# Optimization experiments

Measured on AMD Instinct MI355X. Metric: run time of the kernel, lower is better.

The kernel has to match this reference:

```python
import jax, jax.numpy as jnp
import numpy as np

H = 16      # num_attention_heads
D = 64      # attention_head_size
HID = H * D # hidden_size = 1024
N = 1024    # seq_len == max_len
K = 1024    # position_buckets == att_span (K >= N so un-clamped indices stay in range)
EPS = 1e-7  # layer_norm_eps


def setup_inputs() -> dict:
    key = jax.random.key(0)
    ks = jax.random.split(key, 12)

    def w(k, shape):
        return jax.random.normal(k, shape, dtype=jnp.float32) * 0.02

    return {
        "hidden_states": jax.random.normal(ks[0], (1, N, HID), dtype=jnp.float32),
        "rel_embeddings": jax.random.normal(ks[1], (2 * K, HID), dtype=jnp.float32),
        "Wq": w(ks[2], (HID, HID)), "bq": jnp.zeros((HID,), jnp.float32),
        "Wk": w(ks[3], (HID, HID)), "bk": jnp.zeros((HID,), jnp.float32),
        "Wv": w(ks[4], (HID, HID)), "bv": jnp.zeros((HID,), jnp.float32),
        "Wpk": w(ks[5], (HID, HID)), "bpk": jnp.zeros((HID,), jnp.float32),
        "Wpq": w(ks[6], (HID, HID)), "bpq": jnp.zeros((HID,), jnp.float32),
        "Wo": w(ks[7], (HID, HID)), "bo": jnp.zeros((HID,), jnp.float32),
        "ln_g": jnp.ones((HID,), jnp.float32),
        "ln_b": jnp.zeros((HID,), jnp.float32),
    }


def _heads(x):
    # (L, HID) -> (H, L, D)   (batch size is 1, matching the baked-in id offsets)
    L = x.shape[0]
    return x.reshape(L, H, D).transpose(1, 0, 2)


def reference(hidden_states, rel_embeddings, Wq, bq, Wk, bk, Wv, bv,
              Wpk, bpk, Wpq, bpq, Wo, bo, ln_g, ln_b):
    hs = hidden_states[0]                       # (N, HID)
    q = _heads(hs @ Wq.T + bq)                  # (H, N, D)
    k = _heads(hs @ Wk.T + bk)                  # (H, N, D)
    v = _heads(hs @ Wv.T + bv)                  # (H, N, D)

    scale = jnp.sqrt(jnp.asarray(D * 3, jnp.float32))  # scale_factor = 1 + c2p + p2c = 3
    scores = jnp.einsum('hid,hjd->hij', q, k) / scale  # (H, N, N)

    pos_k = _heads(rel_embeddings @ Wpk.T + bpk)       # (H, 2K, D)
    pos_q = _heads(rel_embeddings @ Wpq.T + bpq)       # (H, 2K, D)

    rows = jnp.arange(N)[:, None]                      # (N, 1)
    # ids[i, j] = (i - j) + K  (no clamp in the original; valid since K >= N)
    idx = K + jnp.arange(N)[:, None] - jnp.arange(N)[None, :]  # (N, N)

    # c2p: gather c2p_att[h, i, K + i - j]
    c2p_att = jnp.einsum('hid,hkd->hik', q, pos_k)     # (H, N, 2K)
    c2p = c2p_att[:, rows, idx]                        # (H, N, N)

    # p2c: gather p2c_att[h, i, K + j - i], then transpose last two dims
    p2c_att = jnp.einsum('hid,hkd->hik', k, pos_q)     # (H, N, 2K)
    p2c = jnp.swapaxes(p2c_att[:, rows, idx.T], -1, -2)  # (H, N, N)

    scores = scores + (c2p + p2c) / scale
    attn = jax.nn.softmax(scores, axis=-1)             # (H, N, N)

    ctx = jnp.einsum('hij,hjd->hid', attn, v)          # (H, N, D)
    ctx = ctx.transpose(1, 0, 2).reshape(1, N, HID)    # (1, N, HID)

    # DebertaV2SelfOutput: dense + residual LayerNorm
    out = ctx @ Wo.T + bo
    x = out + hidden_states
    mu = jnp.mean(x, axis=-1, keepdims=True)
    var = jnp.mean(jnp.square(x - mu), axis=-1, keepdims=True)
    return ((x - mu) / jnp.sqrt(var + EPS)) * ln_g + ln_b
```

## Files before the change

### kernel.cpp

```cpp
#include <hip/hip_runtime.h>
#include <stdint.h>

#define HID 1024
#define NSEQ 1024
#define KREL 1024
#define NHEAD 16
#define DHEAD 64

typedef __attribute__((ext_vector_type(8))) short bhalf8;
typedef __attribute__((ext_vector_type(4))) float floatx4;

__device__ inline uint16_t f2bf(float f) {
  union { float f; uint32_t u; } c; c.f = f;
  uint32_t u = c.u;
  return (uint16_t)((u + 0x7fffu + ((u >> 16) & 1u)) >> 16);
}
__device__ inline uint32_t pkbf(float a, float b) {
  union { float f; uint32_t u; } x, y; x.f = a; y.f = b;
#if __has_builtin(__builtin_amdgcn_perm)
  return __builtin_amdgcn_perm(x.u + 0x8000u, y.u + 0x8000u, 0x03020706u);
#else
  return ((x.u + 0x8000u) >> 16) | ((y.u + 0x8000u) & 0xffff0000u);
#endif
}

struct ProjArgs {
  const float* A[5];
  const float* W[5];
  const float* bias[5];
  uint16_t* C[5];
  int trans[5];
};
__global__ __launch_bounds__(256) void proj_gemm(ProjArgs pa) {
  __shared__ uint16_t a_s[2][128 * 40];
  __shared__ uint16_t b_s[2][64 * 40];
  int bidx = blockIdx.x;
  int xcd = bidx & 7, idx = bidx >> 3;
  int gl = idx >> 4, nt = idx & 15;
  int g = xcd * 7 + gl;
  int z, mt;
  if (g < 24) { z = g >> 3; mt = g & 7; }
  else { int g2 = g - 24; z = 3 + (g2 >> 4); mt = g2 & 15; }
  const float* A = pa.A[z];
  const float* W = pa.W[z];
  int i0 = mt * 128, n0 = nt * 64;

  int t = threadIdx.x;
  int lane = t & 63, w = t >> 6;
  int fm = lane & 15, kq = lane >> 4;
  int wrow = w * 32;

  int ra = t >> 1, ca = (t & 1) * 16;
  int rb = t >> 2, cbc = (t & 3) * 8;
  const float* Ap = A + (size_t)(i0 + ra) * HID + ca;
  const float* Wp = W + (size_t)(n0 + rb) * HID + cbc;

  floatx4 acc[2][4] = {};

  float4 fa0 = *(const float4*)(Ap);
  float4 fa1 = *(const float4*)(Ap + 4);
  float4 fa2 = *(const float4*)(Ap + 8);
  float4 fa3 = *(const float4*)(Ap + 12);
  float4 fb0 = *(const float4*)(Wp);
  float4 fb1 = *(const float4*)(Wp + 4);
  {
    uint4 u0 = { pkbf(fa0.x,fa0.y), pkbf(fa0.z,fa0.w), pkbf(fa1.x,fa1.y), pkbf(fa1.z,fa1.w) };
    uint4 u1 = { pkbf(fa2.x,fa2.y), pkbf(fa2.z,fa2.w), pkbf(fa3.x,fa3.y), pkbf(fa3.z,fa3.w) };
    *(uint4*)(&a_s[0][ra * 40 + ca]) = u0;
    *(uint4*)(&a_s[0][ra * 40 + ca + 8]) = u1;
    uint4 ub = { pkbf(fb0.x,fb0.y), pkbf(fb0.z,fb0.w), pkbf(fb1.x,fb1.y), pkbf(fb1.z,fb1.w) };
    *(uint4*)(&b_s[0][rb * 40 + cbc]) = ub;
  }

  for (int kt = 0; kt < 32; ++kt) {
    __syncthreads();
    int cur = kt & 1;
    if (kt < 31) {
      int ko = (kt + 1) * 32;
      fa0 = *(const float4*)(Ap + ko);
      fa1 = *(const float4*)(Ap + ko + 4);
      fa2 = *(const float4*)(Ap + ko + 8);
      fa3 = *(const float4*)(Ap + ko + 12);
      fb0 = *(const float4*)(Wp + ko);
      fb1 = *(const float4*)(Wp + ko + 4);
    }
    const uint16_t* as = &a_s[cur][0];
    const uint16_t* bs = &b_s[cur][0];
    bhalf8 af[2], bfr[4];
#pragma unroll
    for (int m2 = 0; m2 < 2; ++m2)
      af[m2] = *(bhalf8*)(as + (wrow + m2 * 16 + fm) * 40 + kq * 8);
#pragma unroll
    for (int n2 = 0; n2 < 4; ++n2)
      bfr[n2] = *(bhalf8*)(bs + (n2 * 16 + fm) * 40 + kq * 8);
#pragma unroll
    for (int m2 = 0; m2 < 2; ++m2)
#pragma unroll
      for (int n2 = 0; n2 < 4; ++n2)
        acc[m2][n2] = __builtin_amdgcn_mfma_f32_16x16x32_bf16(af[m2], bfr[n2], acc[m2][n2], 0, 0, 0);
    if (kt < 31) {
      int nxt = cur ^ 1;
      uint4 u0 = { pkbf(fa0.x,fa0.y), pkbf(fa0.z,fa0.w), pkbf(fa1.x,fa1.y), pkbf(fa1.z,fa1.w) };
      uint4 u1 = { pkbf(fa2.x,fa2.y), pkbf(fa2.z,fa2.w), pkbf(fa3.x,fa3.y), pkbf(fa3.z,fa3.w) };
      *(uint4*)(&a_s[nxt][ra * 40 + ca]) = u0;
      *(uint4*)(&a_s[nxt][ra * 40 + ca + 8]) = u1;
      uint4 ub = { pkbf(fb0.x,fb0.y), pkbf(fb0.z,fb0.w), pkbf(fb1.x,fb1.y), pkbf(fb1.z,fb1.w) };
      *(uint4*)(&b_s[nxt][rb * 40 + cbc]) = ub;
    }
  }

  const float* bias = pa.bias[z];
  uint16_t* C = pa.C[z];
  int tr = pa.trans[z];
#pragma unroll
  for (int m2 = 0; m2 < 2; ++m2) {
    int rowb = i0 + wrow + m2 * 16 + kq * 4;
#pragma unroll
    for (int n2 = 0; n2 < 4; ++n2) {
      int col = n0 + n2 * 16 + fm;
      float bv = bias[col];
      floatx4 v = acc[m2][n2];
      if (tr) {
        uint2 p = { pkbf(v[0] + bv, v[1] + bv), pkbf(v[2] + bv, v[3] + bv) };
        *(uint2*)(C + (size_t)col * NSEQ + rowb) = p;
      } else {
#pragma unroll
        for (int r = 0; r < 4; ++r)
          C[(size_t)(rowb + r) * HID + col] = f2bf(v[r] + bv);
      }
    }
  }
}

__global__ __launch_bounds__(256) void out_gemm(const uint16_t* __restrict__ Abf,
                                                const float* __restrict__ W,
                                                const float* __restrict__ bias,
                                                float* __restrict__ C) {
  __shared__ uint16_t a_s[2][128 * 40];
  __shared__ uint16_t b_s[2][64 * 40];
  int bidx = blockIdx.x;
  int mt = bidx >> 4, nt = bidx & 15;
  int i0 = mt * 128, n0 = nt * 64;
  int t = threadIdx.x;
  int lane = t & 63, w = t >> 6;
  int fm = lane & 15, kq = lane >> 4;
  int wrow = w * 32;
  int ra = t >> 1, ca = (t & 1) * 16;
  int rb = t >> 2, cbc = (t & 3) * 8;
  const uint16_t* Ap = Abf + (size_t)(i0 + ra) * HID + ca;
  const float* Wp = W + (size_t)(n0 + rb) * HID + cbc;
  floatx4 acc[2][4] = {};
  uint4 va0 = *(const uint4*)(Ap);
  uint4 va1 = *(const uint4*)(Ap + 8);
  float4 fb0 = *(const float4*)(Wp);
  float4 fb1 = *(const float4*)(Wp + 4);
  *(uint4*)(&a_s[0][ra * 40 + ca]) = va0;
  *(uint4*)(&a_s[0][ra * 40 + ca + 8]) = va1;
  {
    uint4 ub = { pkbf(fb0.x,fb0.y), pkbf(fb0.z,fb0.w), pkbf(fb1.x,fb1.y), pkbf(fb1.z,fb1.w) };
    *(uint4*)(&b_s[0][rb * 40 + cbc]) = ub;
  }
  for (int kt = 0; kt < 32; ++kt) {
    __syncthreads();
    int cur = kt & 1;
    if (kt < 31) {
      int ko = (kt + 1) * 32;
      va0 = *(const uint4*)(Ap + ko);
      va1 = *(const uint4*)(Ap + ko + 8);
      fb0 = *(const float4*)(Wp + ko);
      fb1 = *(const float4*)(Wp + ko + 4);
    }
    const uint16_t* as = &a_s[cur][0];
    const uint16_t* bs = &b_s[cur][0];
    bhalf8 af[2], bfr[4];
#pragma unroll
    for (int m2 = 0; m2 < 2; ++m2)
      af[m2] = *(bhalf8*)(as + (wrow + m2 * 16 + fm) * 40 + kq * 8);
#pragma unroll
    for (int n2 = 0; n2 < 4; ++n2)
      bfr[n2] = *(bhalf8*)(bs + (n2 * 16 + fm) * 40 + kq * 8);
#pragma unroll
    for (int m2 = 0; m2 < 2; ++m2)
#pragma unroll
      for (int n2 = 0; n2 < 4; ++n2)
        acc[m2][n2] = __builtin_amdgcn_mfma_f32_16x16x32_bf16(af[m2], bfr[n2], acc[m2][n2], 0, 0, 0);
    if (kt < 31) {
      int nxt = cur ^ 1;
      *(uint4*)(&a_s[nxt][ra * 40 + ca]) = va0;
      *(uint4*)(&a_s[nxt][ra * 40 + ca + 8]) = va1;
      uint4 ub = { pkbf(fb0.x,fb0.y), pkbf(fb0.z,fb0.w), pkbf(fb1.x,fb1.y), pkbf(fb1.z,fb1.w) };
      *(uint4*)(&b_s[nxt][rb * 40 + cbc]) = ub;
    }
  }
#pragma unroll
  for (int m2 = 0; m2 < 2; ++m2) {
    int rowb = i0 + wrow + m2 * 16 + kq * 4;
#pragma unroll
    for (int n2 = 0; n2 < 4; ++n2) {
      int col = n0 + n2 * 16 + fm;
      float bv = bias[col];
#pragma unroll
      for (int r = 0; r < 4; ++r)
        C[(size_t)(rowb + r) * HID + col] = acc[m2][n2][r] + bv;
    }
  }
}

__global__ __launch_bounds__(256) void attn_kernel(const uint16_t* __restrict__ qg,
                                                   const uint16_t* __restrict__ kg,
                                                   const uint16_t* __restrict__ vtg,
                                                   const uint16_t* __restrict__ pkg,
                                                   const uint16_t* __restrict__ pqg,
                                                   uint16_t* __restrict__ ctx) {
  const float RSCALE = 0.07216878364870323f;
  __shared__ uint16_t Qs[32][72];
  __shared__ uint16_t Ks[32][72];
  __shared__ uint16_t Vt[64][40];
  __shared__ uint16_t PKw[64][72];
  __shared__ uint16_t PQw[64][72];
  __shared__ float C2P[32][68];
  __shared__ float P2C[32][68];
  __shared__ float Sqk[32][36];
  __shared__ uint16_t Pbf[32][40];
  __shared__ float m_sm[32], l_sm[32], al_sm[32];

  int t = threadIdx.x;
  int lane = t & 63, w = t >> 6;
  int fm = lane & 15;
  int kq = lane >> 4;

  int b = blockIdx.x;
  int xcd = b & 7, slot = b >> 3;
  int h = xcd * 2 + (slot & 1);
  int i0 = (slot >> 1) * 32;
  int cb = h * DHEAD;

  {
    int r = t >> 3, chq = (t & 7) * 8;
    *(uint4*)(&Qs[r][chq]) = *(const uint4*)(qg + (size_t)(i0 + r) * HID + cb + chq);
  }
  if (t < 32) { m_sm[t] = -1e30f; l_sm[t] = 0.f; }

  floatx4 opv0 = {0,0,0,0}, opv1 = {0,0,0,0};
  int wn = w * 16;
  int smt = w >> 1, snt = w & 1;
  int i2 = t >> 3, jj = t & 7;

  int pr = t >> 3, pch = (t & 7) * 8;
  int rV = t >> 2, cV = (t & 3) * 8;
  const uint16_t* kb = kg + cb + pch;
  const uint16_t* vb = vtg + (size_t)(cb + rV) * HID + cV;
  const uint16_t* pkb = pkg + cb + pch;
  const uint16_t* pqb = pqg + cb + pch;

  uint4 rk, rv, rpk0, rpk1, rpq0, rpq1;
  {
    int j0 = 0;
    int rbase = KREL + i0 - j0 - 31;
    rk = *(const uint4*)(kb + (size_t)(j0 + pr) * HID);
    rv = *(const uint4*)(vb + j0);
    int rg0 = rbase + pr;
    int rg1 = rbase + pr + 32; if (rg1 > 2047) rg1 = 2047;
    rpk0 = *(const uint4*)(pkb + (size_t)rg0 * HID);
    rpk1 = *(const uint4*)(pkb + (size_t)rg1 * HID);
    rpq0 = *(const uint4*)(pqb + (size_t)rg0 * HID);
    rpq1 = *(const uint4*)(pqb + (size_t)rg1 * HID);
  }

  for (int jt = 0; jt < NSEQ / 32; ++jt) {
    __syncthreads();
    *(uint4*)(&Ks[pr][pch]) = rk;
    *(uint4*)(&Vt[rV][cV]) = rv;
    *(uint4*)(&PKw[pr][pch]) = rpk0;
    *(uint4*)(&PKw[pr + 32][pch]) = rpk1;
    *(uint4*)(&PQw[pr][pch]) = rpq0;
    *(uint4*)(&PQw[pr + 32][pch]) = rpq1;
    __syncthreads();

    if (jt + 1 < NSEQ / 32) {
      int j0 = (jt + 1) * 32;
      int rbase = KREL + i0 - j0 - 31;
      rk = *(const uint4*)(kb + (size_t)(j0 + pr) * HID);
      rv = *(const uint4*)(vb + j0);
      int rg0 = rbase + pr; if (rg0 < 0) rg0 = 0;
      int rg1 = rbase + pr + 32; if (rg1 > 2047) rg1 = 2047;
      rpk0 = *(const uint4*)(pkb + (size_t)rg0 * HID);
      rpk1 = *(const uint4*)(pkb + (size_t)rg1 * HID);
      rpq0 = *(const uint4*)(pqb + (size_t)rg0 * HID);
      rpq1 = *(const uint4*)(pqb + (size_t)rg1 * HID);
    }

    {
      const uint16_t* Asrc = (w < 2) ? &Qs[0][0] : &Ks[0][0];
      const uint16_t* Bsrc = (w < 2) ? &PKw[0][0] : &PQw[0][0];
      float* Cdst = (w < 2) ? &C2P[0][0] : &P2C[0][0];
      int ntb = (w & 1) * 2;
#pragma unroll
      for (int mt = 0; mt < 2; ++mt) {
        bhalf8 a0 = *(bhalf8*)(Asrc + (mt * 16 + fm) * 72 + kq * 8);
        bhalf8 a1 = *(bhalf8*)(Asrc + (mt * 16 + fm) * 72 + kq * 8 + 32);
#pragma unroll
        for (int nt = ntb; nt < ntb + 2; ++nt) {
          bhalf8 b0 = *(bhalf8*)(Bsrc + (nt * 16 + fm) * 72 + kq * 8);
          bhalf8 b1 = *(bhalf8*)(Bsrc + (nt * 16 + fm) * 72 + kq * 8 + 32);
          floatx4 acc = {0,0,0,0};
          acc = __builtin_amdgcn_mfma_f32_16x16x32_bf16(a0, b0, acc, 0, 0, 0);
          acc = __builtin_amdgcn_mfma_f32_16x16x32_bf16(a1, b1, acc, 0, 0, 0);
#pragma unroll
          for (int r = 0; r < 4; ++r)
            Cdst[(mt * 16 + kq * 4 + r) * 68 + nt * 16 + fm] = acc[r];
        }
      }
      bhalf8 qa0 = *(bhalf8*)(&Qs[smt * 16 + fm][kq * 8]);
      bhalf8 qa1 = *(bhalf8*)(&Qs[smt * 16 + fm][kq * 8 + 32]);
      bhalf8 kb0 = *(bhalf8*)(&Ks[snt * 16 + fm][kq * 8]);
      bhalf8 kb1 = *(bhalf8*)(&Ks[snt * 16 + fm][kq * 8 + 32]);
      floatx4 sacc = {0,0,0,0};
      sacc = __builtin_amdgcn_mfma_f32_16x16x32_bf16(qa0, kb0, sacc, 0, 0, 0);
      sacc = __builtin_amdgcn_mfma_f32_16x16x32_bf16(qa1, kb1, sacc, 0, 0, 0);
#pragma unroll
      for (int r = 0; r < 4; ++r)
        Sqk[smt * 16 + kq * 4 + r][snt * 16 + fm] = sacc[r];
    }
    __syncthreads();

    {
      float sv[4];
#pragma unroll
      for (int q = 0; q < 4; ++q) {
        int j = jj + 8 * q;
        int rr = i2 - j + 31;
        sv[q] = (Sqk[i2][j] + C2P[i2][rr] + P2C[j][rr]) * RSCALE;
      }
      float mx = fmaxf(fmaxf(sv[0], sv[1]), fmaxf(sv[2], sv[3]));
      mx = fmaxf(mx, __shfl_xor(mx, 1));
      mx = fmaxf(mx, __shfl_xor(mx, 2));
      mx = fmaxf(mx, __shfl_xor(mx, 4));
      float m_old = m_sm[i2];
      float m_new = fmaxf(m_old, mx);
      float al = __expf(m_old - m_new);
      float ts = 0.f;
#pragma unroll
      for (int q = 0; q < 4; ++q) {
        float e = __expf(sv[q] - m_new);
        Pbf[i2][jj + 8 * q] = f2bf(e);
        ts += e;
      }
      ts += __shfl_xor(ts, 1);
      ts += __shfl_xor(ts, 2);
      ts += __shfl_xor(ts, 4);
      if (jj == 0) { m_sm[i2] = m_new; l_sm[i2] = l_sm[i2] * al + ts; al_sm[i2] = al; }
    }
    __syncthreads();

    {
#pragma unroll
      for (int r = 0; r < 4; ++r) {
        opv0[r] *= al_sm[kq * 4 + r];
        opv1[r] *= al_sm[16 + kq * 4 + r];
      }
      bhalf8 vbf = *(bhalf8*)(&Vt[wn + fm][kq * 8]);
      bhalf8 pa0 = *(bhalf8*)(&Pbf[fm][kq * 8]);
      bhalf8 pa1 = *(bhalf8*)(&Pbf[16 + fm][kq * 8]);
      opv0 = __builtin_amdgcn_mfma_f32_16x16x32_bf16(pa0, vbf, opv0, 0, 0, 0);
      opv1 = __builtin_amdgcn_mfma_f32_16x16x32_bf16(pa1, vbf, opv1, 0, 0, 0);
    }
  }

#pragma unroll
  for (int r = 0; r < 4; ++r) {
    int ia = kq * 4 + r, ib = 16 + kq * 4 + r;
    float la = 1.0f / l_sm[ia], lb = 1.0f / l_sm[ib];
    ctx[(size_t)(i0 + ia) * HID + cb + wn + fm] = f2bf(opv0[r] * la);
    ctx[(size_t)(i0 + ib) * HID + cb + wn + fm] = f2bf(opv1[r] * lb);
  }
}

__global__ __launch_bounds__(256) void ln_kernel(const float* __restrict__ xin,
                                                 const float* __restrict__ hs,
                                                 const float* __restrict__ g,
                                                 const float* __restrict__ b,
                                                 float* __restrict__ y) {
  int row = blockIdx.x, t = threadIdx.x;
  int c = t * 4;
  float4 a = *(const float4*)(xin + (size_t)row * HID + c);
  float4 hv = *(const float4*)(hs + (size_t)row * HID + c);
  float x0 = a.x + hv.x, x1 = a.y + hv.y, x2 = a.z + hv.z, x3 = a.w + hv.w;
  float s = x0 + x1 + x2 + x3;
  float sq = x0 * x0 + x1 * x1 + x2 * x2 + x3 * x3;
  for (int off = 32; off; off >>= 1) {
    s += __shfl_xor(s, off);
    sq += __shfl_xor(sq, off);
  }
  __shared__ float rs[4], rq[4];
  int w = t >> 6, lane = t & 63;
  if (lane == 0) { rs[w] = s; rq[w] = sq; }
  __syncthreads();
  s = rs[0] + rs[1] + rs[2] + rs[3];
  sq = rq[0] + rq[1] + rq[2] + rq[3];
  float mu = s * (1.0f / HID);
  float var = sq * (1.0f / HID) - mu * mu;
  float rstd = rsqrtf(var + 1e-7f);
  float4 gg = *(const float4*)(g + c);
  float4 bb = *(const float4*)(b + c);
  float4 out;
  out.x = (x0 - mu) * rstd * gg.x + bb.x;
  out.y = (x1 - mu) * rstd * gg.y + bb.y;
  out.z = (x2 - mu) * rstd * gg.z + bb.z;
  out.w = (x3 - mu) * rstd * gg.w + bb.w;
  *(float4*)(y + (size_t)row * HID + c) = out;
}

extern "C" void kernel_launch(void* const* d_in, const int* in_sizes, int n_in,
                              void* d_out, int out_size, void* d_ws, size_t ws_size,
                              hipStream_t stream) {
  const float* hs  = (const float*)d_in[0];
  const float* rel = (const float*)d_in[1];
  const float* Wq  = (const float*)d_in[2];  const float* bq  = (const float*)d_in[3];
  const float* Wk  = (const float*)d_in[4];  const float* bk  = (const float*)d_in[5];
  const float* Wv  = (const float*)d_in[6];  const float* bv  = (const float*)d_in[7];
  const float* Wpk = (const float*)d_in[8];  const float* bpk = (const float*)d_in[9];
  const float* Wpq = (const float*)d_in[10]; const float* bpq = (const float*)d_in[11];
  const float* Wo  = (const float*)d_in[12]; const float* bo  = (const float*)d_in[13];
  const float* lng = (const float*)d_in[14]; const float* lnb = (const float*)d_in[15];

  char* ws = (char*)d_ws;
  const size_t MB = 1024 * 1024;
  uint16_t* q_bf   = (uint16_t*)(ws + 0 * MB);
  uint16_t* k_bf   = (uint16_t*)(ws + 2 * MB);
  uint16_t* vt_bf  = (uint16_t*)(ws + 4 * MB);
  uint16_t* pk_bf  = (uint16_t*)(ws + 6 * MB);
  uint16_t* pq_bf  = (uint16_t*)(ws + 10 * MB);
  uint16_t* ctx_bf = (uint16_t*)(ws + 14 * MB);
  float*    out_f  = (float*)   (ws + 16 * MB);

  dim3 blk(256);

  ProjArgs pa;
  pa.A[0] = hs;  pa.A[1] = hs;  pa.A[2] = hs;  pa.A[3] = rel; pa.A[4] = rel;
  pa.W[0] = Wq;  pa.W[1] = Wk;  pa.W[2] = Wv;  pa.W[3] = Wpk; pa.W[4] = Wpq;
  pa.bias[0] = bq;  pa.bias[1] = bk;  pa.bias[2] = bv;  pa.bias[3] = bpk; pa.bias[4] = bpq;
  pa.C[0] = q_bf; pa.C[1] = k_bf; pa.C[2] = vt_bf; pa.C[3] = pk_bf; pa.C[4] = pq_bf;
  pa.trans[0] = 0; pa.trans[1] = 0; pa.trans[2] = 1; pa.trans[3] = 0; pa.trans[4] = 0;
  proj_gemm<<<dim3(896), blk, 0, stream>>>(pa);

  attn_kernel<<<dim3(512), blk, 0, stream>>>(q_bf, k_bf, vt_bf, pk_bf, pq_bf, ctx_bf);

  out_gemm<<<dim3(128), blk, 0, stream>>>(ctx_bf, Wo, bo, out_f);

  ln_kernel<<<dim3(1024), blk, 0, stream>>>(out_f, hs, lng, lnb, (float*)d_out);
}
```

Baseline: 235.7 us.

## Pre-cast inputs and weights to bf16, retile out_gemm, store rel-pos scores in bf16

Adds one cast kernel that converts hidden states, rel embeddings and all six weight matrices to bf16 in workspace, so the projection and output GEMMs load bf16 directly instead of converting fp32 in their inner loops. The output GEMM is retiled to 64x64 blocks with a 2x2 warp layout, doubling its grid from 128 to 256 blocks. The attention kernel keeps C2P/P2C tiles in bf16 shared memory, halving that LDS footprint. The extra cast pass adds a launch and about 40MB of memory traffic every call, and the bf16 position scores lose precision.

```diff
diff --git a/kernel.cpp b/kernel.cpp
--- a/kernel.cpp
+++ b/kernel.cpp
@@ -10,6 +10,9 @@
 typedef __attribute__((ext_vector_type(8))) short bhalf8;
 typedef __attribute__((ext_vector_type(4))) float floatx4;
 
+__device__ inline float bf2f(uint16_t h) {
+  union { uint32_t u; float f; } c; c.u = ((uint32_t)h) << 16; return c.f;
+}
 __device__ inline uint16_t f2bf(float f) {
   union { float f; uint32_t u; } c; c.f = f;
   uint32_t u = c.u;
@@ -24,9 +27,27 @@
 #endif
 }
 
+struct Cast8 {
+  const float* src[8];
+  uint16_t* dst[8];
+  int n[8];
+};
+__global__ __launch_bounds__(256) void cast8_kernel(Cast8 c) {
+  int seg = blockIdx.y;
+  int n = c.n[seg];
+  const float* s = c.src[seg];
+  uint16_t* d = c.dst[seg];
+  for (int idx = (blockIdx.x * 256 + threadIdx.x) * 4; idx < n; idx += 1024 * 256 * 4) {
+    float4 v = *(const float4*)(s + idx);
+    ushort4 o;
+    o.x = f2bf(v.x); o.y = f2bf(v.y); o.z = f2bf(v.z); o.w = f2bf(v.w);
+    *(ushort4*)(d + idx) = o;
+  }
+}
+
 struct ProjArgs {
-  const float* A[5];
-  const float* W[5];
+  const uint16_t* A[5];
+  const uint16_t* W[5];
   const float* bias[5];
   uint16_t* C[5];
   int trans[5];
@@ -41,8 +62,8 @@
   int z, mt;
   if (g < 24) { z = g >> 3; mt = g & 7; }
   else { int g2 = g - 24; z = 3 + (g2 >> 4); mt = g2 & 15; }
-  const float* A = pa.A[z];
-  const float* W = pa.W[z];
+  const uint16_t* A = pa.A[z];
+  const uint16_t* W = pa.W[z];
   int i0 = mt * 128, n0 = nt * 64;
 
   int t = threadIdx.x;
@@ -52,37 +73,26 @@
 
   int ra = t >> 1, ca = (t & 1) * 16;
   int rb = t >> 2, cbc = (t & 3) * 8;
-  const float* Ap = A + (size_t)(i0 + ra) * HID + ca;
-  const float* Wp = W + (size_t)(n0 + rb) * HID + cbc;
+  const uint16_t* Ap = A + (size_t)(i0 + ra) * HID + ca;
+  const uint16_t* Wp = W + (size_t)(n0 + rb) * HID + cbc;
 
   floatx4 acc[2][4] = {};
 
-  float4 fa0 = *(const float4*)(Ap);
-  float4 fa1 = *(const float4*)(Ap + 4);
-  float4 fa2 = *(const float4*)(Ap + 8);
-  float4 fa3 = *(const float4*)(Ap + 12);
-  float4 fb0 = *(const float4*)(Wp);
-  float4 fb1 = *(const float4*)(Wp + 4);
-  {
-    uint4 u0 = { pkbf(fa0.x,fa0.y), pkbf(fa0.z,fa0.w), pkbf(fa1.x,fa1.y), pkbf(fa1.z,fa1.w) };
-    uint4 u1 = { pkbf(fa2.x,fa2.y), pkbf(fa2.z,fa2.w), pkbf(fa3.x,fa3.y), pkbf(fa3.z,fa3.w) };
-    *(uint4*)(&a_s[0][ra * 40 + ca]) = u0;
-    *(uint4*)(&a_s[0][ra * 40 + ca + 8]) = u1;
-    uint4 ub = { pkbf(fb0.x,fb0.y), pkbf(fb0.z,fb0.w), pkbf(fb1.x,fb1.y), pkbf(fb1.z,fb1.w) };
-    *(uint4*)(&b_s[0][rb * 40 + cbc]) = ub;
-  }
+  uint4 ua0 = *(const uint4*)(Ap);
+  uint4 ua1 = *(const uint4*)(Ap + 8);
+  uint4 ub = *(const uint4*)(Wp);
+  *(uint4*)(&a_s[0][ra * 40 + ca]) = ua0;
+  *(uint4*)(&a_s[0][ra * 40 + ca + 8]) = ua1;
+  *(uint4*)(&b_s[0][rb * 40 + cbc]) = ub;
 
   for (int kt = 0; kt < 32; ++kt) {
     __syncthreads();
     int cur = kt & 1;
     if (kt < 31) {
       int ko = (kt + 1) * 32;
-      fa0 = *(const float4*)(Ap + ko);
-      fa1 = *(const float4*)(Ap + ko + 4);
-      fa2 = *(const float4*)(Ap + ko + 8);
-      fa3 = *(const float4*)(Ap + ko + 12);
-      fb0 = *(const float4*)(Wp + ko);
-      fb1 = *(const float4*)(Wp + ko + 4);
+      ua0 = *(const uint4*)(Ap + ko);
+      ua1 = *(const uint4*)(Ap + ko + 8);
+      ub = *(const uint4*)(Wp + ko);
     }
     const uint16_t* as = &a_s[cur][0];
     const uint16_t* bs = &b_s[cur][0];
@@ -100,11 +110,8 @@
         acc[m2][n2] = __builtin_amdgcn_mfma_f32_16x16x32_bf16(af[m2], bfr[n2], acc[m2][n2], 0, 0, 0);
     if (kt < 31) {
       int nxt = cur ^ 1;
-      uint4 u0 = { pkbf(fa0.x,fa0.y), pkbf(fa0.z,fa0.w), pkbf(fa1.x,fa1.y), pkbf(fa1.z,fa1.w) };
-      uint4 u1 = { pkbf(fa2.x,fa2.y), pkbf(fa2.z,fa2.w), pkbf(fa3.x,fa3.y), pkbf(fa3.z,fa3.w) };
-      *(uint4*)(&a_s[nxt][ra * 40 + ca]) = u0;
-      *(uint4*)(&a_s[nxt][ra * 40 + ca + 8]) = u1;
-      uint4 ub = { pkbf(fb0.x,fb0.y), pkbf(fb0.z,fb0.w), pkbf(fb1.x,fb1.y), pkbf(fb1.z,fb1.w) };
+      *(uint4*)(&a_s[nxt][ra * 40 + ca]) = ua0;
+      *(uint4*)(&a_s[nxt][ra * 40 + ca + 8]) = ua1;
       *(uint4*)(&b_s[nxt][rb * 40 + cbc]) = ub;
     }
   }
@@ -133,77 +140,61 @@
 }
 
 __global__ __launch_bounds__(256) void out_gemm(const uint16_t* __restrict__ Abf,
-                                                const float* __restrict__ W,
+                                                const uint16_t* __restrict__ W,
                                                 const float* __restrict__ bias,
                                                 float* __restrict__ C) {
-  __shared__ uint16_t a_s[2][128 * 40];
+  __shared__ uint16_t a_s[2][64 * 40];
   __shared__ uint16_t b_s[2][64 * 40];
   int bidx = blockIdx.x;
-  int mt = bidx >> 4, nt = bidx & 15;
-  int i0 = mt * 128, n0 = nt * 64;
+  int i0 = (bidx >> 4) * 64, n0 = (bidx & 15) * 64;
   int t = threadIdx.x;
   int lane = t & 63, w = t >> 6;
   int fm = lane & 15, kq = lane >> 4;
-  int wrow = w * 32;
-  int ra = t >> 1, ca = (t & 1) * 16;
-  int rb = t >> 2, cbc = (t & 3) * 8;
+  int wm = (w >> 1) * 32, wn = (w & 1) * 32;
+  int ra = t >> 2, ca = (t & 3) * 8;
   const uint16_t* Ap = Abf + (size_t)(i0 + ra) * HID + ca;
-  const float* Wp = W + (size_t)(n0 + rb) * HID + cbc;
-  floatx4 acc[2][4] = {};
-  uint4 va0 = *(const uint4*)(Ap);
-  uint4 va1 = *(const uint4*)(Ap + 8);
-  float4 fb0 = *(const float4*)(Wp);
-  float4 fb1 = *(const float4*)(Wp + 4);
-  *(uint4*)(&a_s[0][ra * 40 + ca]) = va0;
-  *(uint4*)(&a_s[0][ra * 40 + ca + 8]) = va1;
-  {
-    uint4 ub = { pkbf(fb0.x,fb0.y), pkbf(fb0.z,fb0.w), pkbf(fb1.x,fb1.y), pkbf(fb1.z,fb1.w) };
-    *(uint4*)(&b_s[0][rb * 40 + cbc]) = ub;
-  }
+  const uint16_t* Wp = W + (size_t)(n0 + ra) * HID + ca;
+  floatx4 acc00 = {0,0,0,0}, acc01 = {0,0,0,0}, acc10 = {0,0,0,0}, acc11 = {0,0,0,0};
+  uint4 ua = *(const uint4*)(Ap);
+  uint4 ub = *(const uint4*)(Wp);
+  *(uint4*)(&a_s[0][ra * 40 + ca]) = ua;
+  *(uint4*)(&b_s[0][ra * 40 + ca]) = ub;
   for (int kt = 0; kt < 32; ++kt) {
     __syncthreads();
     int cur = kt & 1;
     if (kt < 31) {
       int ko = (kt + 1) * 32;
-      va0 = *(const uint4*)(Ap + ko);
-      va1 = *(const uint4*)(Ap + ko + 8);
-      fb0 = *(const float4*)(Wp + ko);
-      fb1 = *(const float4*)(Wp + ko + 4);
+      ua = *(const uint4*)(Ap + ko);
+      ub = *(const uint4*)(Wp + ko);
     }
     const uint16_t* as = &a_s[cur][0];
     const uint16_t* bs = &b_s[cur][0];
-    bhalf8 af[2], bfr[4];
-#pragma unroll
-    for (int m2 = 0; m2 < 2; ++m2)
-      af[m2] = *(bhalf8*)(as + (wrow + m2 * 16 + fm) * 40 + kq * 8);
-#pragma unroll
-    for (int n2 = 0; n2 < 4; ++n2)
-      bfr[n2] = *(bhalf8*)(bs + (n2 * 16 + fm) * 40 + kq * 8);
-#pragma unroll
-    for (int m2 = 0; m2 < 2; ++m2)
-#pragma unroll
-      for (int n2 = 0; n2 < 4; ++n2)
-        acc[m2][n2] = __builtin_amdgcn_mfma_f32_16x16x32_bf16(af[m2], bfr[n2], acc[m2][n2], 0, 0, 0);
+    bhalf8 a0 = *(bhalf8*)(as + (wm + fm) * 40 + kq * 8);
+    bhalf8 a1 = *(bhalf8*)(as + (wm + 16 + fm) * 40 + kq * 8);
+    bhalf8 b0 = *(bhalf8*)(bs + (wn + fm) * 40 + kq * 8);
+    bhalf8 b1 = *(bhalf8*)(bs + (wn + 16 + fm) * 40 + kq * 8);
+    acc00 = __builtin_amdgcn_mfma_f32_16x16x32_bf16(a0, b0, acc00, 0, 0, 0);
+    acc01 = __builtin_amdgcn_mfma_f32_16x16x32_bf16(a0, b1, acc01, 0, 0, 0);
+    acc10 = __builtin_amdgcn_mfma_f32_16x16x32_bf16(a1, b0, acc10, 0, 0, 0);
+    acc11 = __builtin_amdgcn_mfma_f32_16x16x32_bf16(a1, b1, acc11, 0, 0, 0);
     if (kt < 31) {
       int nxt = cur ^ 1;
-      *(uint4*)(&a_s[nxt][ra * 40 + ca]) = va0;
-      *(uint4*)(&a_s[nxt][ra * 40 + ca + 8]) = va1;
-      uint4 ub = { pkbf(fb0.x,fb0.y), pkbf(fb0.z,fb0.w), pkbf(fb1.x,fb1.y), pkbf(fb1.z,fb1.w) };
-      *(uint4*)(&b_s[nxt][rb * 40 + cbc]) = ub;
-    }
-  }
-#pragma unroll
-  for (int m2 = 0; m2 < 2; ++m2) {
-    int rowb = i0 + wrow + m2 * 16 + kq * 4;
-#pragma unroll
-    for (int n2 = 0; n2 < 4; ++n2) {
-      int col = n0 + n2 * 16 + fm;
-      float bv = bias[col];
-#pragma unroll
-      for (int r = 0; r < 4; ++r)
-        C[(size_t)(rowb + r) * HID + col] = acc[m2][n2][r] + bv;
-    }
-  }
+      *(uint4*)(&a_s[nxt][ra * 40 + ca]) = ua;
+      *(uint4*)(&b_s[nxt][ra * 40 + ca]) = ub;
+    }
+  }
+  int rb0 = kq * 4;
+#define EPO(ACC, SM, SN)                                                   \
+  {                                                                        \
+    int rowb = i0 + wm + (SM)*16 + rb0;                                    \
+    int col = n0 + wn + (SN)*16 + fm;                                      \
+    float bv_ = bias[col];                                                 \
+    _Pragma("unroll")                                                      \
+    for (int rr = 0; rr < 4; ++rr)                                         \
+      C[(size_t)(rowb + rr) * HID + col] = ACC[rr] + bv_;                  \
+  }
+  EPO(acc00, 0, 0) EPO(acc01, 0, 1) EPO(acc10, 1, 0) EPO(acc11, 1, 1)
+#undef EPO
 }
 
 __global__ __launch_bounds__(256) void attn_kernel(const uint16_t* __restrict__ qg,
@@ -218,8 +209,8 @@
   __shared__ uint16_t Vt[64][40];
   __shared__ uint16_t PKw[64][72];
   __shared__ uint16_t PQw[64][72];
-  __shared__ float C2P[32][68];
-  __shared__ float P2C[32][68];
+  __shared__ uint16_t C2P[32][68];
+  __shared__ uint16_t P2C[32][68];
   __shared__ float Sqk[32][36];
   __shared__ uint16_t Pbf[32][40];
   __shared__ float m_sm[32], l_sm[32], al_sm[32];
@@ -293,7 +284,7 @@
     {
       const uint16_t* Asrc = (w < 2) ? &Qs[0][0] : &Ks[0][0];
       const uint16_t* Bsrc = (w < 2) ? &PKw[0][0] : &PQw[0][0];
-      float* Cdst = (w < 2) ? &C2P[0][0] : &P2C[0][0];
+      uint16_t* Cdst = (w < 2) ? &C2P[0][0] : &P2C[0][0];
       int ntb = (w & 1) * 2;
 #pragma unroll
       for (int mt = 0; mt < 2; ++mt) {
@@ -308,7 +299,7 @@
           acc = __builtin_amdgcn_mfma_f32_16x16x32_bf16(a1, b1, acc, 0, 0, 0);
 #pragma unroll
           for (int r = 0; r < 4; ++r)
-            Cdst[(mt * 16 + kq * 4 + r) * 68 + nt * 16 + fm] = acc[r];
+            Cdst[(mt * 16 + kq * 4 + r) * 68 + nt * 16 + fm] = f2bf(acc[r]);
         }
       }
       bhalf8 qa0 = *(bhalf8*)(&Qs[smt * 16 + fm][kq * 8]);
@@ -330,7 +321,7 @@
       for (int q = 0; q < 4; ++q) {
         int j = jj + 8 * q;
         int rr = i2 - j + 31;
-        sv[q] = (Sqk[i2][j] + C2P[i2][rr] + P2C[j][rr]) * RSCALE;
+        sv[q] = (Sqk[i2][j] + bf2f(C2P[i2][rr]) + bf2f(P2C[j][rr])) * RSCALE;
       }
       float mx = fmaxf(fmaxf(sv[0], sv[1]), fmaxf(sv[2], sv[3]));
       mx = fmaxf(mx, __shfl_xor(mx, 1));
@@ -433,12 +424,31 @@
   uint16_t* pq_bf  = (uint16_t*)(ws + 10 * MB);
   uint16_t* ctx_bf = (uint16_t*)(ws + 14 * MB);
   float*    out_f  = (float*)   (ws + 16 * MB);
+  uint16_t* hs_bf  = (uint16_t*)(ws + 20 * MB);
+  uint16_t* rel_bf = (uint16_t*)(ws + 22 * MB);
+  uint16_t* Wq_bf  = (uint16_t*)(ws + 26 * MB);
+  uint16_t* Wk_bf  = (uint16_t*)(ws + 28 * MB);
+  uint16_t* Wv_bf  = (uint16_t*)(ws + 30 * MB);
+  uint16_t* Wpk_bf = (uint16_t*)(ws + 32 * MB);
+  uint16_t* Wpq_bf = (uint16_t*)(ws + 34 * MB);
+  uint16_t* Wo_bf  = (uint16_t*)(ws + 36 * MB);
 
   dim3 blk(256);
 
+  Cast8 c8;
+  c8.src[0] = hs;  c8.dst[0] = hs_bf;  c8.n[0] = 1024 * 1024;
+  c8.src[1] = rel; c8.dst[1] = rel_bf; c8.n[1] = 2048 * 1024;
+  c8.src[2] = Wq;  c8.dst[2] = Wq_bf;  c8.n[2] = 1024 * 1024;
+  c8.src[3] = Wk;  c8.dst[3] = Wk_bf;  c8.n[3] = 1024 * 1024;
+  c8.src[4] = Wv;  c8.dst[4] = Wv_bf;  c8.n[4] = 1024 * 1024;
+  c8.src[5] = Wpk; c8.dst[5] = Wpk_bf; c8.n[5] = 1024 * 1024;
+  c8.src[6] = Wpq; c8.dst[6] = Wpq_bf; c8.n[6] = 1024 * 1024;
+  c8.src[7] = Wo;  c8.dst[7] = Wo_bf;  c8.n[7] = 1024 * 1024;
+  cast8_kernel<<<dim3(1024, 8), blk, 0, stream>>>(c8);
+
   ProjArgs pa;
-  pa.A[0] = hs;  pa.A[1] = hs;  pa.A[2] = hs;  pa.A[3] = rel; pa.A[4] = rel;
-  pa.W[0] = Wq;  pa.W[1] = Wk;  pa.W[2] = Wv;  pa.W[3] = Wpk; pa.W[4] = Wpq;
+  pa.A[0] = hs_bf;  pa.A[1] = hs_bf;  pa.A[2] = hs_bf;  pa.A[3] = rel_bf; pa.A[4] = rel_bf;
+  pa.W[0] = Wq_bf;  pa.W[1] = Wk_bf;  pa.W[2] = Wv_bf;  pa.W[3] = Wpk_bf; pa.W[4] = Wpq_bf;
   pa.bias[0] = bq;  pa.bias[1] = bk;  pa.bias[2] = bv;  pa.bias[3] = bpk; pa.bias[4] = bpq;
   pa.C[0] = q_bf; pa.C[1] = k_bf; pa.C[2] = vt_bf; pa.C[3] = pk_bf; pa.C[4] = pq_bf;
   pa.trans[0] = 0; pa.trans[1] = 0; pa.trans[2] = 1; pa.trans[3] = 0; pa.trans[4] = 0;
@@ -446,7 +456,7 @@
 
   attn_kernel<<<dim3(512), blk, 0, stream>>>(q_bf, k_bf, vt_bf, pk_bf, pq_bf, ctx_bf);
 
-  out_gemm<<<dim3(128), blk, 0, stream>>>(ctx_bf, Wo, bo, out_f);
+  out_gemm<<<dim3(256), blk, 0, stream>>>(ctx_bf, Wo_bf, bo, out_f);
 
   ln_kernel<<<dim3(1024), blk, 0, stream>>>(out_f, hs, lng, lnb, (float*)d_out);
 }
```

After: 209.5 us. -11.1%, faster.
